# Kernel tuning notes

Hardware: AMD Instinct MI355X
Metric: run time of the kernel (lower is better)

Reference implementation:

```python
import jax, jax.numpy as jnp
import numpy as np

S, B, D, L = 100, 2048, 128, 2  # seq_len, batch, dim_model, n_layers
LN_EPS = 1e-5


def _layer_norm(x, g, b):
    # x: [S, B, D]; normalize over last dim (nn.LayerNorm(dim))
    mu = jnp.mean(x, axis=-1, keepdims=True)
    var = jnp.mean(jnp.square(x - mu), axis=-1, keepdims=True)
    return (x - mu) * jax.lax.rsqrt(var + LN_EPS) * g + b


def _asb(x, cw, cwh, thr):
    # Adaptive_Spectral_Block. x: [S, B, D] -> permute to [B, N, C]
    xb = jnp.transpose(x, (1, 0, 2)).astype(jnp.float32)  # [B, N, C]
    N = xb.shape[1]
    x_fft = jnp.fft.rfft(xb, axis=1, norm='ortho')  # [B, F, C] complex, F = N//2+1
    w = jax.lax.complex(cw[:, 0], cw[:, 1])          # [C]
    x_weighted = x_fft * w
    # adaptive high-frequency mask
    energy = jnp.sum(jnp.square(jnp.abs(x_fft)), axis=-1)  # [B, F]
    F = energy.shape[1]
    # torch.median returns the LOWER of the two middle values -> k-th smallest, k=(F-1)//2
    median = jnp.sort(energy, axis=1)[:, (F - 1) // 2][:, None]  # [B, 1]
    norm_e = energy / (median + 1e-6)
    threshold = jnp.quantile(norm_e, thr)  # global scalar quantile (linear interp, as torch)
    mask = (norm_e < threshold)[..., None].astype(x_fft.real.dtype)  # [B, F, 1]
    wh = jax.lax.complex(cwh[:, 0], cwh[:, 1])       # [C]
    x_weighted = x_weighted + (x_fft * mask) * wh
    out = jnp.fft.irfft(x_weighted, n=N, axis=1, norm='ortho')  # [B, N, C]
    return jnp.transpose(out, (1, 0, 2)).astype(x.dtype)  # back to [S, B, D]


def setup_inputs() -> dict:
    key = jax.random.key(0)
    k0, k1, k2, k3 = jax.random.split(key, 4)
    return {
        'x': jax.random.normal(k0, (S, B, D), dtype=jnp.float32),
        'complex_weight': jax.random.normal(k1, (L, D, 2), dtype=jnp.float32) * 0.02,
        'complex_weight_high': jax.random.normal(k2, (L, D, 2), dtype=jnp.float32) * 0.02,
        'threshold_param': jax.random.uniform(k3, (L,), dtype=jnp.float32) * 0.5,
        'gamma': jnp.ones((L, D), dtype=jnp.float32),
        'beta': jnp.zeros((L, D), dtype=jnp.float32),
    }


def reference(x, complex_weight, complex_weight_high, threshold_param, gamma, beta):
    # Encoder.forward: nlayers x (x = x + ASB(LayerNorm(x)))
    for i in range(L):
        h = _layer_norm(x, gamma[i], beta[i])
        x = x + _asb(h, complex_weight[i], complex_weight_high[i], threshold_param[i])
    return x
```

## Files before the change

### kernel.cpp

```cpp
#include <hip/hip_runtime.h>
#include <math.h>

#define SEQ    100
#define BATCH  2048
#define DIM    128
#define NF     51
#define NLAYER 2
#define MTOT   (BATCH * NF)
#define BD     (BATCH * DIM)
#define XSTR   16384

typedef __attribute__((ext_vector_type(8))) short bf16x8;
typedef __attribute__((ext_vector_type(4))) float f32x4v;

__device__ __forceinline__ unsigned short f2bf(float f) {
    unsigned u = __float_as_uint(f);
    return (unsigned short)((u + 0x7FFFu + ((u >> 16) & 1u)) >> 16);
}
__device__ __forceinline__ float bf2f(unsigned short u) {
    return __uint_as_float((unsigned)u << 16);
}

__global__ void k_tables(unsigned short* __restrict__ imgF,
                         unsigned short* __restrict__ imgI) {
    const int i = blockIdx.x * 256 + threadIdx.x;
    const float W = 6.28318530717958647692f / 100.f;
    if (i < 2 * 64 * 128) {
        const int p = i >> 13, k = (i >> 7) & 63, n = i & 127;
        float v = 0.f;
        if (k < NF && n < SEQ) {
            float s, c; sincosf((float)((k * n) % 100) * W, &s, &c);
            v = 0.1f * (p ? -s : c);
        }
        imgF[i] = f2bf(v);
    }
    if (i < 2 * 128 * 64) {
        const int p = i >> 13, n = (i >> 6) & 127, k = i & 63;
        float v = 0.f;
        if (k < NF && n < SEQ) {
            float s, c; sincosf((float)((k * n) % 100) * W, &s, &c);
            const float a = (k == 0 || k == 50) ? 0.1f : 0.2f;
            v = p ? -a * s : a * c;
        }
        imgI[i] = f2bf(v);
    }
}

__global__ __launch_bounds__(256, 4) void k_fwd(
    const float* __restrict__ x,
    const float* __restrict__ gamma, const float* __restrict__ beta,
    const unsigned short* __restrict__ imgF,
    unsigned short* __restrict__ Xg,
    float* __restrict__ normE)
{
    __shared__ __align__(16) unsigned short hT[128 * 128];
    __shared__ float epart[64][4];
    __shared__ float energy_s[64];
    __shared__ float med_s;

    const int b = blockIdx.x, t = threadIdx.x;
    const int lane = t & 63, wv = t >> 6, g4 = lane >> 4, cc = lane & 15;

    {
        const int c0 = lane * 2;
        const float2 gv = *(const float2*)&gamma[c0];
        const float2 bv = *(const float2*)&beta[c0];
        float2 v[4][8];
        #pragma unroll
        for (int slot = 0; slot < 4; ++slot) {
            const int n0 = (slot * 4 + wv) * 8;
            #pragma unroll
            for (int j = 0; j < 8; ++j)
                if (n0 + j < SEQ)
                    v[slot][j] = *(const float2*)&x[(size_t)(n0 + j) * BD + (size_t)b * DIM + c0];
        }
        #pragma unroll
        for (int slot = 0; slot < 4; ++slot) {
            const int chunk = slot * 4 + wv;
            const int n0 = chunk * 8;
            unsigned we[4], wo[4];
            #pragma unroll
            for (int j = 0; j < 8; ++j) {
                unsigned short he = 0, ho = 0;
                if (n0 + j < SEQ) {
                    float s  = v[slot][j].x + v[slot][j].y;
                    float s2 = fmaf(v[slot][j].x, v[slot][j].x, v[slot][j].y * v[slot][j].y);
                    #pragma unroll
                    for (int off = 1; off < 64; off <<= 1) {
                        s  += __shfl_xor(s,  off, 64);
                        s2 += __shfl_xor(s2, off, 64);
                    }
                    const float mu   = s * (1.f / 128.f);
                    const float rstd = rsqrtf(s2 * (1.f / 128.f) - mu * mu + 1e-5f);
                    he = f2bf(fmaf((v[slot][j].x - mu) * rstd, gv.x, bv.x));
                    ho = f2bf(fmaf((v[slot][j].y - mu) * rstd, gv.y, bv.y));
                }
                if (j & 1) { we[j >> 1] |= (unsigned)he << 16; wo[j >> 1] |= (unsigned)ho << 16; }
                else       { we[j >> 1]  = he;                 wo[j >> 1]  = ho; }
            }
            const int sw = (chunk ^ (lane & 7)) << 3;
            int4 ve; ve.x = (int)we[0]; ve.y = (int)we[1]; ve.z = (int)we[2]; ve.w = (int)we[3];
            int4 vo; vo.x = (int)wo[0]; vo.y = (int)wo[1]; vo.z = (int)wo[2]; vo.w = (int)wo[3];
            *(int4*)&hT[(c0    ) * 128 + sw] = ve;
            *(int4*)&hT[(c0 + 1) * 128 + sw] = vo;
        }
    }
    __syncthreads();

    bf16x8 Bf[2][4];
    #pragma unroll
    for (int ct = 0; ct < 2; ++ct) {
        const int c = wv * 32 + ct * 16 + cc;
        #pragma unroll
        for (int ks = 0; ks < 4; ++ks)
            Bf[ct][ks] = *(const bf16x8*)&hT[c * 128 + (((ks * 4 + g4) ^ (cc >> 1)) << 3)];
    }

    #pragma unroll
    for (int mt = 0; mt < 4; ++mt) {
        const int kr = mt * 16 + cc;
        f32x4v aR[2], aI[2];
        aR[0] = aR[1] = aI[0] = aI[1] = (f32x4v){0.f, 0.f, 0.f, 0.f};
        #pragma unroll
        for (int ks = 0; ks < 4; ++ks) {
            const int e0 = kr * 128 + ks * 32 + g4 * 8;
            const bf16x8 A0 = *(const bf16x8*)&imgF[e0];
            const bf16x8 A1 = *(const bf16x8*)&imgF[8192 + e0];
            #pragma unroll
            for (int ct = 0; ct < 2; ++ct) {
                aR[ct] = __builtin_amdgcn_mfma_f32_16x16x32_bf16(A0, Bf[ct][ks], aR[ct], 0, 0, 0);
                aI[ct] = __builtin_amdgcn_mfma_f32_16x16x32_bf16(A1, Bf[ct][ks], aI[ct], 0, 0, 0);
            }
        }
        #pragma unroll
        for (int reg = 0; reg < 4; ++reg) {
            float e = aR[0][reg] * aR[0][reg] + aI[0][reg] * aI[0][reg]
                    + aR[1][reg] * aR[1][reg] + aI[1][reg] * aI[1][reg];
            e += __shfl_xor(e, 1, 64); e += __shfl_xor(e, 2, 64);
            e += __shfl_xor(e, 4, 64); e += __shfl_xor(e, 8, 64);
            if (cc == 0) epart[mt * 16 + g4 * 4 + reg][wv] = e;
        }
        #pragma unroll
        for (int ct = 0; ct < 2; ++ct) {
            const int c = wv * 32 + ct * 16 + cc;
            unsigned short* Xb = Xg + (size_t)b * XSTR + (size_t)c * 128;
            const int k0 = mt * 16 + g4 * 4;
            uint2 pr, pi;
            pr.x = (unsigned)f2bf(aR[ct][0]) | ((unsigned)f2bf(aR[ct][1]) << 16);
            pr.y = (unsigned)f2bf(aR[ct][2]) | ((unsigned)f2bf(aR[ct][3]) << 16);
            pi.x = (unsigned)f2bf(aI[ct][0]) | ((unsigned)f2bf(aI[ct][1]) << 16);
            pi.y = (unsigned)f2bf(aI[ct][2]) | ((unsigned)f2bf(aI[ct][3]) << 16);
            *(uint2*)&Xb[k0]      = pr;
            *(uint2*)&Xb[64 + k0] = pi;
        }
    }
    __syncthreads();
    if (t < 64) energy_s[t] = epart[t][0] + epart[t][1] + epart[t][2] + epart[t][3];
    __syncthreads();
    if (t < NF) {
        const float e = energy_s[t];
        int cnt = 0;
        for (int j = 0; j < NF; ++j) {
            const float ej = energy_s[j];
            cnt += (ej < e || (ej == e && j < t)) ? 1 : 0;
        }
        if (cnt == (NF - 1) / 2) med_s = e;
    }
    __syncthreads();
    if (t < NF) normE[b * NF + t] = energy_s[t] / (med_s + 1e-6f);
}

__global__ void k_hist0(const float* __restrict__ normE,
                        unsigned* __restrict__ hist)
{
    __shared__ unsigned lh[2048];
    for (int i = threadIdx.x; i < 2048; i += 256) lh[i] = 0;
    __syncthreads();
    for (int i = blockIdx.x * 256 + threadIdx.x; i < MTOT; i += gridDim.x * 256)
        atomicAdd(&lh[__float_as_uint(normE[i]) >> 21], 1u);
    __syncthreads();
    for (int i = threadIdx.x; i < 2048; i += 256) {
        const unsigned c = lh[i];
        if (c) atomicAdd(&hist[i], c);
    }
}

__global__ void k_sel(const float* __restrict__ normE,
                      unsigned* __restrict__ hist,
                      unsigned* __restrict__ sel,
                      unsigned* __restrict__ done,
                      const float* __restrict__ thrp,
                      const int layer, const int phase,
                      float* __restrict__ thresh)
{
    __shared__ unsigned lh[4096];
    __shared__ unsigned sp[2], sc[2];
    __shared__ unsigned ticket_s;
    __shared__ float vb[2];
    const int t = threadIdx.x;
    const float q = thrp[layer] * (float)(MTOT - 1);
    const unsigned r0 = (unsigned)floorf(q);

    if (phase == 1) {
        if (t < 128) {
            const int j = t >> 6, ln = t & 63;
            const unsigned rk = r0 + (unsigned)j;
            unsigned sum = 0;
            for (int i = 0; i < 32; ++i) sum += hist[ln * 32 + i];
            unsigned pre = sum;
            #pragma unroll
            for (int off = 1; off < 64; off <<= 1) {
                const unsigned tt = __shfl_up(pre, off, 64);
                if (ln >= off) pre += tt;
            }
            const unsigned excl = pre - sum;
            if (rk >= excl && rk < excl + sum) {
                unsigned cum = excl;
                for (int i = 0; i < 32; ++i) {
                    const unsigned hc = hist[ln * 32 + i];
                    if (rk < cum + hc) { sp[j] = (unsigned)(ln * 32 + i) << 21; sc[j] = cum; break; }
                    cum += hc;
                }
            }
        }
    } else {
        if (t < 2) { sp[t] = sel[2 * t]; sc[t] = sel[2 * t + 1]; }
    }
    __syncthreads();
    const unsigned p0 = sp[0], p1 = sp[1];
    const int bins      = (phase == 1) ? 2048 : 1024;
    const int shift     = (phase == 1) ? 10 : 0;
    const unsigned hmsk = (phase == 1) ? 0xFFE00000u : 0xFFFFFC00u;
    const int region    = (phase == 1) ? 2048 : 6144;

    for (int i = t; i < 2 * bins; i += 256) lh[i] = 0;
    __syncthreads();
    for (int i = blockIdx.x * 256 + t; i < MTOT; i += gridDim.x * 256) {
        const unsigned v = __float_as_uint(normE[i]);
        const unsigned bin = (v >> shift) & (unsigned)(bins - 1);
        if ((v & hmsk) == p0) atomicAdd(&lh[bin], 1u);
        if ((v & hmsk) == p1) atomicAdd(&lh[bins + bin], 1u);
    }
    __syncthreads();
    for (int i = t; i < 2 * bins; i += 256) {
        const unsigned c = lh[i];
        if (c) atomicAdd(&hist[region + i], c);
    }
    __threadfence();
    if (t == 0) ticket_s = atomicAdd(&done[(layer << 1) + (phase - 1)], 1u);
    __syncthreads();
    if (ticket_s != (unsigned)(gridDim.x - 1)) return;
    __threadfence();

    if (t < 128) {
        const int j = t >> 6, ln = t & 63;
        const unsigned rk  = r0 + (unsigned)j;
        const unsigned rem = rk - sc[j];
        const unsigned* H  = hist + region + j * bins;
        const int per = bins / 64;
        unsigned sum = 0;
        for (int i = 0; i < per; ++i)
            sum += __hip_atomic_load(&H[ln * per + i], __ATOMIC_RELAXED, __HIP_MEMORY_SCOPE_AGENT);
        unsigned pre = sum;
        #pragma unroll
        for (int off = 1; off < 64; off <<= 1) {
            const unsigned tt = __shfl_up(pre, off, 64);
            if (ln >= off) pre += tt;
        }
        const unsigned excl = pre - sum;
        if (rem >= excl && rem < excl + sum) {
            unsigned cum = excl;
            for (int i = 0; i < per; ++i) {
                const unsigned hc = __hip_atomic_load(&H[ln * per + i],
                                        __ATOMIC_RELAXED, __HIP_MEMORY_SCOPE_AGENT);
                if (rem < cum + hc) {
                    const unsigned bin = (unsigned)(ln * per + i);
                    if (phase == 1) { sel[2 * j] = sp[j] | (bin << 10); sel[2 * j + 1] = sc[j] + cum; }
                    else            vb[j] = __uint_as_float(sp[j] | bin);
                    break;
                }
                cum += hc;
            }
        }
    }
    __syncthreads();
    if (phase == 1) { for (int i = t; i < 6144; i += 256) hist[i] = 0u; }
    else            { for (int i = t; i < 2048; i += 256) hist[6144 + i] = 0u; }
    if (t == 0) {
        done[(layer << 1) + (phase - 1)] = 0u;
        if (phase == 2) {
            const float frac = q - floorf(q);
            thresh[0] = vb[0] * (1.f - frac) + vb[1] * frac;
        }
    }
}

__global__ __launch_bounds__(256, 4) void k_asb(
    const float* __restrict__ x,
    const float* __restrict__ cw, const float* __restrict__ cwh,
    const unsigned short* __restrict__ Xg,
    const unsigned short* __restrict__ imgI,
    const float* __restrict__ normE, const float* __restrict__ thresh,
    float* __restrict__ out)
{
    __shared__ float mask_s[64];

    const int b = blockIdx.x, t = threadIdx.x;
    const int lane = t & 63, wv = t >> 6, g4 = lane >> 4, cc = lane & 15;

    if (t < 64) mask_s[t] = (t < NF && normE[b * NF + t] < thresh[0]) ? 1.f : 0.f;
    __syncthreads();

    bf16x8 Yr[2][2], Yi[2][2];
    #pragma unroll
    for (int ct = 0; ct < 2; ++ct) {
        const int c = wv * 32 + ct * 16 + cc;
        const unsigned short* Xb = Xg + (size_t)b * XSTR + (size_t)c * 128;
        const float2 w2 = *(const float2*)&cw[2 * c];
        const float2 h2 = *(const float2*)&cwh[2 * c];
        #pragma unroll
        for (int kb = 0; kb < 2; ++kb) {
            const bf16x8 xr = *(const bf16x8*)&Xb[kb * 32 + g4 * 8];
            const bf16x8 xi = *(const bf16x8*)&Xb[64 + kb * 32 + g4 * 8];
            bf16x8 yr, yi;
            #pragma unroll
            for (int j = 0; j < 8; ++j) {
                const float m   = mask_s[kb * 32 + g4 * 8 + j];
                const float fre = fmaf(m, h2.x, w2.x);
                const float fim = fmaf(m, h2.y, w2.y);
                const float fxr = bf2f((unsigned short)xr[j]);
                const float fxi = bf2f((unsigned short)xi[j]);
                yr[j] = (short)f2bf(fxr * fre - fxi * fim);
                yi[j] = (short)f2bf(fxr * fim + fxi * fre);
            }
            Yr[ct][kb] = yr; Yi[ct][kb] = yi;
        }
    }

    #pragma unroll
    for (int mt = 0; mt < 7; ++mt) {
        const int nr = mt * 16 + cc;
        f32x4v o[2];
        o[0] = o[1] = (f32x4v){0.f, 0.f, 0.f, 0.f};
        #pragma unroll
        for (int kb = 0; kb < 2; ++kb) {
            const int e0 = nr * 64 + kb * 32 + g4 * 8;
            const bf16x8 A0 = *(const bf16x8*)&imgI[e0];
            const bf16x8 A1 = *(const bf16x8*)&imgI[8192 + e0];
            #pragma unroll
            for (int ct = 0; ct < 2; ++ct) {
                o[ct] = __builtin_amdgcn_mfma_f32_16x16x32_bf16(A0, Yr[ct][kb], o[ct], 0, 0, 0);
                o[ct] = __builtin_amdgcn_mfma_f32_16x16x32_bf16(A1, Yi[ct][kb], o[ct], 0, 0, 0);
            }
        }
        #pragma unroll
        for (int ct = 0; ct < 2; ++ct) {
            const int c = wv * 32 + ct * 16 + cc;
            #pragma unroll
            for (int reg = 0; reg < 4; ++reg) {
                const int n = mt * 16 + g4 * 4 + reg;
                if (n < SEQ) {
                    const size_t idx = (size_t)n * BD + (size_t)b * DIM + c;
                    out[idx] = x[idx] + o[ct][reg];
                }
            }
        }
    }
}

extern "C" void kernel_launch(void* const* d_in, const int* in_sizes, int n_in,
                              void* d_out, int out_size, void* d_ws, size_t ws_size,
                              hipStream_t stream)
{
    (void)in_sizes; (void)n_in; (void)out_size; (void)ws_size;
    const float* x    = (const float*)d_in[0];
    const float* cw   = (const float*)d_in[1];
    const float* cwh  = (const float*)d_in[2];
    const float* thrp = (const float*)d_in[3];
    const float* gam  = (const float*)d_in[4];
    const float* bet  = (const float*)d_in[5];
    float* out = (float*)d_out;

    char* ws = (char*)d_ws;
    unsigned short* imgF = (unsigned short*)(ws);
    unsigned short* imgI = (unsigned short*)(ws + 32768);
    unsigned short* Xg   = (unsigned short*)(ws + 65536);
    float* normE   = (float*)(ws + 65536 + 67108864);
    unsigned* hist = (unsigned*)(ws + 65536 + 67108864 + 417792);
    unsigned* done = (unsigned*)(ws + 65536 + 67108864 + 417792 + 32768);
    unsigned* sel  = (unsigned*)(ws + 65536 + 67108864 + 417792 + 32768 + 64);
    float* thresh  = (float*)(ws + 65536 + 67108864 + 417792 + 32768 + 128);

    k_tables<<<64, 256, 0, stream>>>(imgF, imgI);
    hipMemsetAsync(hist, 0, 32768 + 64, stream);

    for (int l = 0; l < NLAYER; ++l) {
        const float* xi = (l == 0) ? x : out;
        k_fwd<<<BATCH, 256, 0, stream>>>(xi, gam + l * DIM, bet + l * DIM,
                                         imgF, Xg, normE);
        k_hist0<<<96, 256, 0, stream>>>(normE, hist);
        k_sel<<<96, 256, 0, stream>>>(normE, hist, sel, done, thrp, l, 1, thresh);
        k_sel<<<96, 256, 0, stream>>>(normE, hist, sel, done, thrp, l, 2, thresh);
        k_asb<<<BATCH, 256, 0, stream>>>(xi, cw + l * DIM * 2, cwh + l * DIM * 2,
                                         Xg, imgI, normE, thresh, out);
    }
}
```

Baseline: 351.6 us.

## Fuse quantile selection kernels with a grid barrier and use packed bf16 conversion

Merges the histogram and two-phase radix select kernels into one persistent kernel with 96 blocks that sync through an atomic grid barrier. This cuts kernel launches and the hist memset per layer. It also replaces the manual bf16 rounding with the v_cvt_pk_bf16_f32 instruction, reuses the hT shared buffer for the energy scratch to cut LDS use, and raises the occupancy hints in launch_bounds. The grid barrier assumes all 96 blocks are resident at once, and the hardware conversion's rounding may differ slightly from the old code.

```diff
diff --git a/kernel.cpp b/kernel.cpp
--- a/kernel.cpp
+++ b/kernel.cpp
@@ -9,10 +9,16 @@
 #define MTOT   (BATCH * NF)
 #define BD     (BATCH * DIM)
 #define XSTR   16384
+#define NBQ    96
 
 typedef __attribute__((ext_vector_type(8))) short bf16x8;
 typedef __attribute__((ext_vector_type(4))) float f32x4v;
 
+__device__ __forceinline__ unsigned cvtpk(float lo, float hi) {
+    unsigned r;
+    asm("v_cvt_pk_bf16_f32 %0, %1, %2" : "=v"(r) : "v"(lo), "v"(hi));
+    return r;
+}
 __device__ __forceinline__ unsigned short f2bf(float f) {
     unsigned u = __float_as_uint(f);
     return (unsigned short)((u + 0x7FFFu + ((u >> 16) & 1u)) >> 16);
@@ -46,7 +52,7 @@
     }
 }
 
-__global__ __launch_bounds__(256, 4) void k_fwd(
+__global__ __launch_bounds__(256, 5) void k_fwd(
     const float* __restrict__ x,
     const float* __restrict__ gamma, const float* __restrict__ beta,
     const unsigned short* __restrict__ imgF,
@@ -54,9 +60,6 @@
     float* __restrict__ normE)
 {
     __shared__ __align__(16) unsigned short hT[128 * 128];
-    __shared__ float epart[64][4];
-    __shared__ float energy_s[64];
-    __shared__ float med_s;
 
     const int b = blockIdx.x, t = threadIdx.x;
     const int lane = t & 63, wv = t >> 6, g4 = lane >> 4, cc = lane & 15;
@@ -78,10 +81,10 @@
         for (int slot = 0; slot < 4; ++slot) {
             const int chunk = slot * 4 + wv;
             const int n0 = chunk * 8;
-            unsigned we[4], wo[4];
+            float he[8], ho[8];
             #pragma unroll
             for (int j = 0; j < 8; ++j) {
-                unsigned short he = 0, ho = 0;
+                he[j] = 0.f; ho[j] = 0.f;
                 if (n0 + j < SEQ) {
                     float s  = v[slot][j].x + v[slot][j].y;
                     float s2 = fmaf(v[slot][j].x, v[slot][j].x, v[slot][j].y * v[slot][j].y);
@@ -92,15 +95,16 @@
                     }
                     const float mu   = s * (1.f / 128.f);
                     const float rstd = rsqrtf(s2 * (1.f / 128.f) - mu * mu + 1e-5f);
-                    he = f2bf(fmaf((v[slot][j].x - mu) * rstd, gv.x, bv.x));
-                    ho = f2bf(fmaf((v[slot][j].y - mu) * rstd, gv.y, bv.y));
+                    he[j] = fmaf((v[slot][j].x - mu) * rstd, gv.x, bv.x);
+                    ho[j] = fmaf((v[slot][j].y - mu) * rstd, gv.y, bv.y);
                 }
-                if (j & 1) { we[j >> 1] |= (unsigned)he << 16; wo[j >> 1] |= (unsigned)ho << 16; }
-                else       { we[j >> 1]  = he;                 wo[j >> 1]  = ho; }
-            }
+            }
+            int4 ve, vo;
+            ve.x = (int)cvtpk(he[0], he[1]); ve.y = (int)cvtpk(he[2], he[3]);
+            ve.z = (int)cvtpk(he[4], he[5]); ve.w = (int)cvtpk(he[6], he[7]);
+            vo.x = (int)cvtpk(ho[0], ho[1]); vo.y = (int)cvtpk(ho[2], ho[3]);
+            vo.z = (int)cvtpk(ho[4], ho[5]); vo.w = (int)cvtpk(ho[6], ho[7]);
             const int sw = (chunk ^ (lane & 7)) << 3;
-            int4 ve; ve.x = (int)we[0]; ve.y = (int)we[1]; ve.z = (int)we[2]; ve.w = (int)we[3];
-            int4 vo; vo.x = (int)wo[0]; vo.y = (int)wo[1]; vo.z = (int)wo[2]; vo.w = (int)wo[3];
             *(int4*)&hT[(c0    ) * 128 + sw] = ve;
             *(int4*)&hT[(c0 + 1) * 128 + sw] = vo;
         }
@@ -115,6 +119,11 @@
         for (int ks = 0; ks < 4; ++ks)
             Bf[ct][ks] = *(const bf16x8*)&hT[c * 128 + (((ks * 4 + g4) ^ (cc >> 1)) << 3)];
     }
+    __syncthreads();
+
+    float* epart    = (float*)hT;
+    float* energy_s = (float*)hT + 256;
+    float* medp     = (float*)hT + 320;
 
     #pragma unroll
     for (int mt = 0; mt < 4; ++mt) {
@@ -138,7 +147,7 @@
                     + aR[1][reg] * aR[1][reg] + aI[1][reg] * aI[1][reg];
             e += __shfl_xor(e, 1, 64); e += __shfl_xor(e, 2, 64);
             e += __shfl_xor(e, 4, 64); e += __shfl_xor(e, 8, 64);
-            if (cc == 0) epart[mt * 16 + g4 * 4 + reg][wv] = e;
+            if (cc == 0) epart[(mt * 16 + g4 * 4 + reg) * 4 + wv] = e;
         }
         #pragma unroll
         for (int ct = 0; ct < 2; ++ct) {
@@ -146,16 +155,15 @@
             unsigned short* Xb = Xg + (size_t)b * XSTR + (size_t)c * 128;
             const int k0 = mt * 16 + g4 * 4;
             uint2 pr, pi;
-            pr.x = (unsigned)f2bf(aR[ct][0]) | ((unsigned)f2bf(aR[ct][1]) << 16);
-            pr.y = (unsigned)f2bf(aR[ct][2]) | ((unsigned)f2bf(aR[ct][3]) << 16);
-            pi.x = (unsigned)f2bf(aI[ct][0]) | ((unsigned)f2bf(aI[ct][1]) << 16);
-            pi.y = (unsigned)f2bf(aI[ct][2]) | ((unsigned)f2bf(aI[ct][3]) << 16);
+            pr.x = cvtpk(aR[ct][0], aR[ct][1]); pr.y = cvtpk(aR[ct][2], aR[ct][3]);
+            pi.x = cvtpk(aI[ct][0], aI[ct][1]); pi.y = cvtpk(aI[ct][2], aI[ct][3]);
             *(uint2*)&Xb[k0]      = pr;
             *(uint2*)&Xb[64 + k0] = pi;
         }
     }
     __syncthreads();
-    if (t < 64) energy_s[t] = epart[t][0] + epart[t][1] + epart[t][2] + epart[t][3];
+    if (t < 64) energy_s[t] = epart[4 * t] + epart[4 * t + 1]
+                            + epart[4 * t + 2] + epart[4 * t + 3];
     __syncthreads();
     if (t < NF) {
         const float e = energy_s[t];
@@ -164,99 +172,35 @@
             const float ej = energy_s[j];
             cnt += (ej < e || (ej == e && j < t)) ? 1 : 0;
         }
-        if (cnt == (NF - 1) / 2) med_s = e;
-    }
-    __syncthreads();
-    if (t < NF) normE[b * NF + t] = energy_s[t] / (med_s + 1e-6f);
-}
-
-__global__ void k_hist0(const float* __restrict__ normE,
-                        unsigned* __restrict__ hist)
+        if (cnt == (NF - 1) / 2) *medp = e;
+    }
+    __syncthreads();
+    if (t < NF) normE[b * NF + t] = energy_s[t] / (*medp + 1e-6f);
+}
+
+__device__ __forceinline__ void gbar(unsigned* counter, unsigned target) {
+    __syncthreads();
+    __threadfence();
+    if (threadIdx.x == 0) {
+        __hip_atomic_fetch_add(counter, 1u, __ATOMIC_ACQ_REL, __HIP_MEMORY_SCOPE_AGENT);
+        while (__hip_atomic_load(counter, __ATOMIC_ACQUIRE, __HIP_MEMORY_SCOPE_AGENT) < target)
+            __builtin_amdgcn_s_sleep(8);
+    }
+    __syncthreads();
+}
+
+__device__ __forceinline__ void scan2(const unsigned* __restrict__ H0,
+                                      int bins, int shift, bool entry,
+                                      unsigned r0, unsigned* sp, unsigned* sc)
 {
-    __shared__ unsigned lh[2048];
-    for (int i = threadIdx.x; i < 2048; i += 256) lh[i] = 0;
-    __syncthreads();
-    for (int i = blockIdx.x * 256 + threadIdx.x; i < MTOT; i += gridDim.x * 256)
-        atomicAdd(&lh[__float_as_uint(normE[i]) >> 21], 1u);
-    __syncthreads();
-    for (int i = threadIdx.x; i < 2048; i += 256) {
-        const unsigned c = lh[i];
-        if (c) atomicAdd(&hist[i], c);
-    }
-}
-
-__global__ void k_sel(const float* __restrict__ normE,
-                      unsigned* __restrict__ hist,
-                      unsigned* __restrict__ sel,
-                      unsigned* __restrict__ done,
-                      const float* __restrict__ thrp,
-                      const int layer, const int phase,
-                      float* __restrict__ thresh)
-{
-    __shared__ unsigned lh[4096];
-    __shared__ unsigned sp[2], sc[2];
-    __shared__ unsigned ticket_s;
-    __shared__ float vb[2];
     const int t = threadIdx.x;
-    const float q = thrp[layer] * (float)(MTOT - 1);
-    const unsigned r0 = (unsigned)floorf(q);
-
-    if (phase == 1) {
-        if (t < 128) {
-            const int j = t >> 6, ln = t & 63;
-            const unsigned rk = r0 + (unsigned)j;
-            unsigned sum = 0;
-            for (int i = 0; i < 32; ++i) sum += hist[ln * 32 + i];
-            unsigned pre = sum;
-            #pragma unroll
-            for (int off = 1; off < 64; off <<= 1) {
-                const unsigned tt = __shfl_up(pre, off, 64);
-                if (ln >= off) pre += tt;
-            }
-            const unsigned excl = pre - sum;
-            if (rk >= excl && rk < excl + sum) {
-                unsigned cum = excl;
-                for (int i = 0; i < 32; ++i) {
-                    const unsigned hc = hist[ln * 32 + i];
-                    if (rk < cum + hc) { sp[j] = (unsigned)(ln * 32 + i) << 21; sc[j] = cum; break; }
-                    cum += hc;
-                }
-            }
-        }
-    } else {
-        if (t < 2) { sp[t] = sel[2 * t]; sc[t] = sel[2 * t + 1]; }
-    }
-    __syncthreads();
-    const unsigned p0 = sp[0], p1 = sp[1];
-    const int bins      = (phase == 1) ? 2048 : 1024;
-    const int shift     = (phase == 1) ? 10 : 0;
-    const unsigned hmsk = (phase == 1) ? 0xFFE00000u : 0xFFFFFC00u;
-    const int region    = (phase == 1) ? 2048 : 6144;
-
-    for (int i = t; i < 2 * bins; i += 256) lh[i] = 0;
-    __syncthreads();
-    for (int i = blockIdx.x * 256 + t; i < MTOT; i += gridDim.x * 256) {
-        const unsigned v = __float_as_uint(normE[i]);
-        const unsigned bin = (v >> shift) & (unsigned)(bins - 1);
-        if ((v & hmsk) == p0) atomicAdd(&lh[bin], 1u);
-        if ((v & hmsk) == p1) atomicAdd(&lh[bins + bin], 1u);
-    }
-    __syncthreads();
-    for (int i = t; i < 2 * bins; i += 256) {
-        const unsigned c = lh[i];
-        if (c) atomicAdd(&hist[region + i], c);
-    }
-    __threadfence();
-    if (t == 0) ticket_s = atomicAdd(&done[(layer << 1) + (phase - 1)], 1u);
-    __syncthreads();
-    if (ticket_s != (unsigned)(gridDim.x - 1)) return;
-    __threadfence();
-
     if (t < 128) {
         const int j = t >> 6, ln = t & 63;
-        const unsigned rk  = r0 + (unsigned)j;
-        const unsigned rem = rk - sc[j];
-        const unsigned* H  = hist + region + j * bins;
+        const unsigned rk = r0 + (unsigned)j;
+        const unsigned oldsp = entry ? sp[j] : 0u;
+        const unsigned oldsc = entry ? sc[j] : 0u;
+        const unsigned rem = rk - oldsc;
+        const unsigned* H = H0 + (entry ? j * bins : 0);
         const int per = bins / 64;
         unsigned sum = 0;
         for (int i = 0; i < per; ++i)
@@ -274,9 +218,8 @@
                 const unsigned hc = __hip_atomic_load(&H[ln * per + i],
                                         __ATOMIC_RELAXED, __HIP_MEMORY_SCOPE_AGENT);
                 if (rem < cum + hc) {
-                    const unsigned bin = (unsigned)(ln * per + i);
-                    if (phase == 1) { sel[2 * j] = sp[j] | (bin << 10); sel[2 * j + 1] = sc[j] + cum; }
-                    else            vb[j] = __uint_as_float(sp[j] | bin);
+                    sp[j] = oldsp | ((unsigned)(ln * per + i) << shift);
+                    sc[j] = oldsc + cum;
                     break;
                 }
                 cum += hc;
@@ -284,18 +227,87 @@
         }
     }
     __syncthreads();
-    if (phase == 1) { for (int i = t; i < 6144; i += 256) hist[i] = 0u; }
-    else            { for (int i = t; i < 2048; i += 256) hist[6144 + i] = 0u; }
-    if (t == 0) {
-        done[(layer << 1) + (phase - 1)] = 0u;
-        if (phase == 2) {
+}
+
+__global__ void k_quant(const float* __restrict__ normE,
+                        unsigned* __restrict__ hist,
+                        unsigned* __restrict__ counter,
+                        const float* __restrict__ thrp,
+                        const int layer,
+                        float* __restrict__ thresh)
+{
+    __shared__ unsigned lh[4096];
+    __shared__ unsigned sp[2], sc[2];
+    const int t = threadIdx.x, bid = blockIdx.x;
+    const float q = thrp[layer] * (float)(MTOT - 1);
+    const unsigned r0 = (unsigned)floorf(q);
+
+    for (int i = bid * 256 + t; i < 8192; i += NBQ * 256) hist[i] = 0u;
+    gbar(counter, NBQ * 1);
+
+    for (int i = t; i < 2048; i += 256) lh[i] = 0;
+    __syncthreads();
+    for (int i = bid * 256 + t; i < MTOT; i += NBQ * 256)
+        atomicAdd(&lh[__float_as_uint(normE[i]) >> 21], 1u);
+    __syncthreads();
+    for (int i = t; i < 2048; i += 256) {
+        const unsigned c = lh[i];
+        if (c) atomicAdd(&hist[i], c);
+    }
+    gbar(counter, NBQ * 2);
+
+    scan2(hist, 2048, 21, false, r0, sp, sc);
+    {
+        const unsigned p0 = sp[0], p1 = sp[1];
+        for (int i = t; i < 4096; i += 256) lh[i] = 0;
+        __syncthreads();
+        for (int i = bid * 256 + t; i < MTOT; i += NBQ * 256) {
+            const unsigned v = __float_as_uint(normE[i]);
+            const unsigned bin = (v >> 10) & 2047u;
+            if ((v & 0xFFE00000u) == p0) atomicAdd(&lh[bin], 1u);
+            if ((v & 0xFFE00000u) == p1) atomicAdd(&lh[2048 + bin], 1u);
+        }
+        __syncthreads();
+        for (int i = t; i < 4096; i += 256) {
+            const unsigned c = lh[i];
+            if (c) atomicAdd(&hist[2048 + i], c);
+        }
+    }
+    gbar(counter, NBQ * 3);
+
+    scan2(hist + 2048, 2048, 10, true, r0, sp, sc);
+    {
+        const unsigned p0 = sp[0], p1 = sp[1];
+        for (int i = t; i < 2048; i += 256) lh[i] = 0;
+        __syncthreads();
+        for (int i = bid * 256 + t; i < MTOT; i += NBQ * 256) {
+            const unsigned v = __float_as_uint(normE[i]);
+            const unsigned bin = v & 1023u;
+            if ((v & 0xFFFFFC00u) == p0) atomicAdd(&lh[bin], 1u);
+            if ((v & 0xFFFFFC00u) == p1) atomicAdd(&lh[1024 + bin], 1u);
+        }
+        __syncthreads();
+        for (int i = t; i < 2048; i += 256) {
+            const unsigned c = lh[i];
+            if (c) atomicAdd(&hist[6144 + i], c);
+        }
+    }
+    gbar(counter, NBQ * 4);
+
+    if (bid == 0) {
+        scan2(hist + 6144, 1024, 0, true, r0, sp, sc);
+        if (t == 0) {
+            const float v0 = __uint_as_float(sp[0]);
+            const float v1 = __uint_as_float(sp[1]);
             const float frac = q - floorf(q);
-            thresh[0] = vb[0] * (1.f - frac) + vb[1] * frac;
-        }
-    }
-}
-
-__global__ __launch_bounds__(256, 4) void k_asb(
+            thresh[0] = v0 * (1.f - frac) + v1 * frac;
+            __threadfence();
+            __hip_atomic_store(counter, 0u, __ATOMIC_RELEASE, __HIP_MEMORY_SCOPE_AGENT);
+        }
+    }
+}
+
+__global__ __launch_bounds__(256, 8) void k_asb(
     const float* __restrict__ x,
     const float* __restrict__ cw, const float* __restrict__ cwh,
     const unsigned short* __restrict__ Xg,
@@ -303,7 +315,7 @@
     const float* __restrict__ normE, const float* __restrict__ thresh,
     float* __restrict__ out)
 {
-    __shared__ float mask_s[64];
+    __shared__ __align__(16) float mask_s[64];
 
     const int b = blockIdx.x, t = threadIdx.x;
     const int lane = t & 63, wv = t >> 6, g4 = lane >> 4, cc = lane & 15;
@@ -322,7 +334,7 @@
         for (int kb = 0; kb < 2; ++kb) {
             const bf16x8 xr = *(const bf16x8*)&Xb[kb * 32 + g4 * 8];
             const bf16x8 xi = *(const bf16x8*)&Xb[64 + kb * 32 + g4 * 8];
-            bf16x8 yr, yi;
+            float yr[8], yi[8];
             #pragma unroll
             for (int j = 0; j < 8; ++j) {
                 const float m   = mask_s[kb * 32 + g4 * 8 + j];
@@ -330,10 +342,17 @@
                 const float fim = fmaf(m, h2.y, w2.y);
                 const float fxr = bf2f((unsigned short)xr[j]);
                 const float fxi = bf2f((unsigned short)xi[j]);
-                yr[j] = (short)f2bf(fxr * fre - fxi * fim);
-                yi[j] = (short)f2bf(fxr * fim + fxi * fre);
-            }
-            Yr[ct][kb] = yr; Yi[ct][kb] = yi;
+                yr[j] = fxr * fre - fxi * fim;
+                yi[j] = fxr * fim + fxi * fre;
+            }
+            unsigned ur[4], ui[4];
+            #pragma unroll
+            for (int jj = 0; jj < 4; ++jj) {
+                ur[jj] = cvtpk(yr[2 * jj], yr[2 * jj + 1]);
+                ui[jj] = cvtpk(yi[2 * jj], yi[2 * jj + 1]);
+            }
+            Yr[ct][kb] = *(bf16x8*)ur;
+            Yi[ct][kb] = *(bf16x8*)ui;
         }
     }
 
@@ -385,22 +404,19 @@
     unsigned short* imgF = (unsigned short*)(ws);
     unsigned short* imgI = (unsigned short*)(ws + 32768);
     unsigned short* Xg   = (unsigned short*)(ws + 65536);
-    float* normE   = (float*)(ws + 65536 + 67108864);
-    unsigned* hist = (unsigned*)(ws + 65536 + 67108864 + 417792);
-    unsigned* done = (unsigned*)(ws + 65536 + 67108864 + 417792 + 32768);
-    unsigned* sel  = (unsigned*)(ws + 65536 + 67108864 + 417792 + 32768 + 64);
-    float* thresh  = (float*)(ws + 65536 + 67108864 + 417792 + 32768 + 128);
+    float* normE      = (float*)(ws + 65536 + 67108864);
+    unsigned* hist    = (unsigned*)(ws + 65536 + 67108864 + 417792);
+    unsigned* counter = (unsigned*)(ws + 65536 + 67108864 + 417792 + 32768);
+    float* thresh     = (float*)(ws + 65536 + 67108864 + 417792 + 32768 + 64);
 
     k_tables<<<64, 256, 0, stream>>>(imgF, imgI);
-    hipMemsetAsync(hist, 0, 32768 + 64, stream);
+    hipMemsetAsync(counter, 0, 64, stream);
 
     for (int l = 0; l < NLAYER; ++l) {
         const float* xi = (l == 0) ? x : out;
         k_fwd<<<BATCH, 256, 0, stream>>>(xi, gam + l * DIM, bet + l * DIM,
                                          imgF, Xg, normE);
-        k_hist0<<<96, 256, 0, stream>>>(normE, hist);
-        k_sel<<<96, 256, 0, stream>>>(normE, hist, sel, done, thrp, l, 1, thresh);
-        k_sel<<<96, 256, 0, stream>>>(normE, hist, sel, done, thrp, l, 2, thresh);
+        k_quant<<<NBQ, 256, 0, stream>>>(normE, hist, counter, thrp, l, thresh);
         k_asb<<<BATCH, 256, 0, stream>>>(xi, cw + l * DIM * 2, cwh + l * DIM * 2,
                                          Xg, imgI, normE, thresh, out);
     }
```

Measured after the change: 524.8 us. +49.3%, slower.
